# Performance work log

Hardware: AMD Instinct MI355X
Metric: run time of the kernel (lower is better)

## Reference

```python
import jax, jax.numpy as jnp
import numpy as np

B, N, E = 8, 20000, 320000
IN_F, EMBED, HIDDEN = 3, 64, 128


def setup_inputs() -> dict:
    key = jax.random.key(0)
    ks = jax.random.split(key, 16)
    w = lambda k, shape: (jax.random.normal(k, shape, jnp.float32) * 0.05)
    return {
        "actions": jax.random.normal(ks[0], (B, N, 2), jnp.float32),
        "node_features": jax.random.normal(ks[1], (B, 1, N), jnp.float32),
        "edge_index": jax.random.randint(ks[2], (B, 2, E), 0, N, dtype=jnp.int64),
        # GINConv 1 MLP: Linear(3, hidden) -> ReLU -> Linear(hidden, embed)
        "c1_w1": w(ks[3], (IN_F, HIDDEN)), "c1_b1": jnp.zeros((HIDDEN,), jnp.float32),
        "c1_w2": w(ks[4], (HIDDEN, EMBED)), "c1_b2": jnp.zeros((EMBED,), jnp.float32),
        # GINConv 2 MLP: Linear(embed, hidden) -> ReLU -> Linear(hidden, embed)
        "c2_w1": w(ks[5], (EMBED, HIDDEN)), "c2_b1": jnp.zeros((HIDDEN,), jnp.float32),
        "c2_w2": w(ks[6], (HIDDEN, EMBED)), "c2_b2": jnp.zeros((EMBED,), jnp.float32),
        # post-pool MLP (num_mlp_layers=1): Linear(embed, hidden)
        "mlp_w": w(ks[7], (EMBED, HIDDEN)), "mlp_b": jnp.zeros((HIDDEN,), jnp.float32),
        # output layer: Linear(hidden, num_nodes)
        "out_w": w(ks[8], (HIDDEN, N)), "out_b": jnp.zeros((N,), jnp.float32),
    }


def _gin_conv(x, src, dst, w1, b1, w2, b2):
    # message = x[src]; aggregate = scatter-sum into dst; eps=0 -> x + agg; then MLP
    num_nodes = x.shape[0]
    agg = jnp.zeros((num_nodes, x.shape[1]), x.dtype).at[dst].add(x[src])
    h = x + agg
    return jax.nn.relu(h @ w1 + b1) @ w2 + b2


def reference(actions, node_features, edge_index,
              c1_w1, c1_b1, c1_w2, c1_b2,
              c2_w1, c2_b1, c2_w2, c2_b2,
              mlp_w, mlp_b, out_w, out_b):
    nf = jnp.squeeze(node_features)                      # [B, N]
    x = jnp.stack((actions[:, :, 0], actions[:, :, 1], nf), axis=2)  # [B, N, 3]
    x = x.reshape(B * N, IN_F)
    # per-batch node-index offsets, then the original's row-major reshape to (2, B*E)
    offs = (jnp.arange(B, dtype=edge_index.dtype) * N)[:, None, None]
    ei = (edge_index + offs).reshape(2, B * E)
    src, dst = ei[0], ei[1]
    # conv layers (eval mode: dropout is identity), outer ReLU after each conv
    x = jax.nn.relu(_gin_conv(x, src, dst, c1_w1, c1_b1, c1_w2, c1_b2))
    x = jax.nn.relu(_gin_conv(x, src, dst, c2_w1, c2_b1, c2_w2, c2_b2))
    # global sum pool: batch ids are contiguous blocks of N nodes
    x = x.reshape(B, N, EMBED).sum(axis=1)               # [B, embed]
    x = jax.nn.relu(x @ mlp_w + mlp_b)                   # [B, hidden]
    return jax.nn.sigmoid(x @ out_w + out_b)             # [B, num_nodes]
```

## Files before the change

kernel.cpp:

```cpp
#include <hip/hip_runtime.h>
#include <cstdint>
#include <cstddef>

#define NBATCH 8
#define NNODE  20000
#define TWO_E  640000
#define NEDGE  2560000
#define BN     160000
#define HN     80000
#define HID    128
#define EMB    64

#define SB     5000
#define SBB    1250
#define NWG    320
#define CHUNK  8000
#define DCAP   80

#define OFF_POOL     0ull
#define ZERO_BYTES   2048ull
#define OFF_CNT      2048ull
#define OFF_TOTAL    6402048ull
#define OFF_BSTART   6422048ull
#define OFF_BINS     6442080ull
#define OFF_AGG1F    16682080ull
#define OFF_AGG2     17642080ull
#define OFF_X1       27882080ull
#define OFF_W1T1     48362080ull
#define OFF_W1HI     48363616ull
#define OFF_W2HI     48380000ull
#define OFF_W1LO     48396384ull
#define OFF_W2LO     48412768ull
#define OFF_V2HI     48429152ull
#define OFF_V2LO     48445536ull
#define OFF_Q        48461920ull

using bf16x8 = __attribute__((ext_vector_type(8))) short;
using f32x4  = __attribute__((ext_vector_type(4))) float;

__device__ __forceinline__ float bf2f(unsigned short u) {
    union { unsigned int i; float f; } v; v.i = ((unsigned int)u) << 16; return v.f;
}
__device__ __forceinline__ unsigned short f2bf(float x) {
    union { float f; unsigned int i; } v; v.f = x;
    unsigned int r = v.i + 0x7FFF + ((v.i >> 16) & 1);
    return (unsigned short)(r >> 16);
}
__device__ __forceinline__ unsigned int addbf2(unsigned int a, unsigned int b) {
    float lo = bf2f((unsigned short)(a & 0xFFFF)) + bf2f((unsigned short)(b & 0xFFFF));
    float hi = bf2f((unsigned short)(a >> 16))    + bf2f((unsigned short)(b >> 16));
    return (unsigned int)f2bf(lo) | ((unsigned int)f2bf(hi) << 16);
}
__device__ __forceinline__ int chunk_of(int b) { return (b & 7) * 40 + (b >> 3); }

__global__ void k_transpose(const float* __restrict__ w1, const float* __restrict__ v2,
                            const float* __restrict__ w2, const float* __restrict__ w2b,
                            float* __restrict__ w1t,
                            unsigned short* __restrict__ v2hi, unsigned short* __restrict__ v2lo,
                            unsigned short* __restrict__ w1hi, unsigned short* __restrict__ w1lo,
                            unsigned short* __restrict__ w2hi, unsigned short* __restrict__ w2lo) {
    int t = blockIdx.x * blockDim.x + threadIdx.x;
    int stride = gridDim.x * blockDim.x;
    for (int i = t; i < 3 * 128; i += stride) {
        int k = i / 128, j = i % 128;
        w1t[j * 3 + k] = w1[i];
    }
    for (int i = t; i < 8192; i += stride) {
        int j = i & 7, l = (i >> 3) & 63, fid = i >> 9;
        int n16 = fid >> 2, ks = fid & 3;
        int n = n16 * 16 + (l & 15), k = ks * 32 + (l >> 4) * 8 + j;
        float w = v2[k * 64 + n];
        unsigned short hi = f2bf(w);
        v2hi[i] = hi;
        v2lo[i] = f2bf(w - bf2f(hi));
    }
    for (int i = t; i < 8192; i += stride) {
        int j = i & 7, l = (i >> 3) & 63, fid = i >> 9;
        int n16 = fid >> 1, ks = fid & 1;
        int n = n16 * 16 + (l & 15), k = ks * 32 + (l >> 4) * 8 + j;
        float w = w2[k * 128 + n];
        unsigned short hi = f2bf(w);
        w1hi[i] = hi;
        w1lo[i] = f2bf(w - bf2f(hi));
    }
    for (int i = t; i < 8192; i += stride) {
        int j = i & 7, l = (i >> 3) & 63, fid = i >> 9;
        int n16 = fid >> 2, ks = fid & 3;
        int n = n16 * 16 + (l & 15), k = ks * 32 + (l >> 4) * 8 + j;
        float w = w2b[k * 64 + n];
        unsigned short hi = f2bf(w);
        w2hi[i] = hi;
        w2lo[i] = f2bf(w - bf2f(hi));
    }
}

__global__ __launch_bounds__(256) void k_hist(const int* __restrict__ ei,
                                              int* __restrict__ cnt) {
    __shared__ int hist[SB];
    int tid = threadIdx.x, w = chunk_of(blockIdx.x);
    for (int b = tid; b < SB; b += 256) hist[b] = 0;
    __syncthreads();
    for (int i = tid; i < CHUNK; i += 256) {
        int ig = w * CHUNK + i;
        int b = ig / TWO_E;
        int j = ig - b * TWO_E;
        int d4 = b * NNODE + ei[(b + 4) * TWO_E + j];
        atomicAdd(&hist[d4 >> 4], 1);
    }
    __syncthreads();
    for (int b = tid; b < SB; b += 256) cnt[w * SB + b] = hist[b];
}

__global__ __launch_bounds__(256) void k_scanA(int* __restrict__ cnt,
                                               int* __restrict__ total) {
    __shared__ int m[NWG][20];
    int tid = threadIdx.x;
    int b0 = blockIdx.x * 20;
    for (int i = tid; i < NWG * 20; i += 256) {
        int r = i / 20, c = i - r * 20;
        m[r][c] = cnt[r * SB + b0 + c];
    }
    __syncthreads();
    if (tid < 20) {
        int s = 0;
#pragma unroll 8
        for (int r = 0; r < NWG; ++r) { int v = m[r][tid]; m[r][tid] = s; s += v; }
        total[b0 + tid] = s;
    }
    __syncthreads();
    for (int i = tid; i < NWG * 20; i += 256) {
        int r = i / 20, c = i - r * 20;
        cnt[r * SB + b0 + c] = m[r][c];
    }
}

__global__ __launch_bounds__(1024) void k_scanB(const int* __restrict__ total,
                                                int* __restrict__ binStart) {
    __shared__ int tmp[1024];
    int tid = threadIdx.x;
    int v[5], c[5], s = 0;
    if (tid < 1000) {
#pragma unroll
        for (int k = 0; k < 5; ++k) v[k] = total[tid * 5 + k];
#pragma unroll
        for (int k = 0; k < 5; ++k) { c[k] = s; s += v[k]; }
    }
    tmp[tid] = s;
    __syncthreads();
    for (int off = 1; off < 1024; off <<= 1) {
        int t = (tid >= off) ? tmp[tid - off] : 0;
        __syncthreads();
        tmp[tid] += t;
        __syncthreads();
    }
    if (tid < 1000) {
        int excl = tmp[tid] - s;
#pragma unroll
        for (int k = 0; k < 5; ++k) binStart[tid * 5 + k] = excl + c[k];
    }
    if (tid == 0) binStart[SB] = NEDGE;
}

__global__ __launch_bounds__(256) void k_place(const int* __restrict__ ei,
                                               const int* __restrict__ cnt,
                                               const int* __restrict__ binStart,
                                               unsigned int* __restrict__ bins) {
    __shared__ int cur[SB];
    int tid = threadIdx.x, w = chunk_of(blockIdx.x);
    for (int b = tid; b < SB; b += 256) cur[b] = binStart[b] + cnt[w * SB + b];
    __syncthreads();
    for (int i = tid; i < CHUNK; i += 256) {
        int ig = w * CHUNK + i;
        int b = ig / TWO_E;
        int j = ig - b * TWO_E;
        int sn = ei[b * TWO_E + j];
        int d4 = b * NNODE + ei[(b + 4) * TWO_E + j];
        unsigned int e = ((unsigned int)d4 << 15) | (unsigned int)sn;
        int pos = atomicAdd(&cur[d4 >> 4], 1);
        bins[pos] = e;
    }
}

__global__ __launch_bounds__(256) void k_agg1(const unsigned int* __restrict__ bins,
                                              const int* __restrict__ binStart,
                                              const float* __restrict__ actions,
                                              const float* __restrict__ nf,
                                              float* __restrict__ agg1f) {
    int tid = threadIdx.x, lane = tid & 63, wv = tid >> 6;
    int sub = blockIdx.x * 4 + wv;
    int dstBase = sub * 16;
    int batchBase = (dstBase / NNODE) * NNODE;
    int start = binStart[sub];
    int cnt = binStart[sub + 1] - start;
    const float2* act2 = reinterpret_cast<const float2*>(actions);

    float acc[48];
#pragma unroll
    for (int k = 0; k < 48; ++k) acc[k] = 0.0f;

    for (int base = 0; base < cnt; base += 64) {
        int i = base + lane;
        float v0 = 0.f, v1 = 0.f, v2 = 0.f;
        int slot = 16;
        if (i < cnt) {
            unsigned int e = bins[start + i];
            slot = (int)((e >> 15) & 15);
            int s = batchBase + (int)(e & 0x7FFF);
            float2 a = act2[s];
            v0 = a.x; v1 = a.y; v2 = nf[s];
        }
#pragma unroll
        for (int t = 0; t < 16; ++t) {
            bool m = (slot == t);
            acc[t * 3 + 0] += m ? v0 : 0.0f;
            acc[t * 3 + 1] += m ? v1 : 0.0f;
            acc[t * 3 + 2] += m ? v2 : 0.0f;
        }
    }

#pragma unroll
    for (int k = 0; k < 48; ++k) {
        float v = acc[k];
        v += __shfl_xor(v, 1, 64);
        v += __shfl_xor(v, 2, 64);
        v += __shfl_xor(v, 4, 64);
        v += __shfl_xor(v, 8, 64);
        v += __shfl_xor(v, 16, 64);
        v += __shfl_xor(v, 32, 64);
        acc[k] = v;
    }
    float outv = 0.0f;
#pragma unroll
    for (int k = 0; k < 48; ++k) outv = (lane == k) ? acc[k] : outv;
    if (lane < 48) agg1f[dstBase * 3 + lane] = outv;
}

__global__ __launch_bounds__(256) void k_conv1(const float* __restrict__ actions,
                                               const float* __restrict__ nf,
                                               const float* __restrict__ agg1f,
                                               const float* __restrict__ w1t,
                                               const float* __restrict__ b1,
                                               const unsigned short* __restrict__ v2hi,
                                               const unsigned short* __restrict__ v2lo,
                                               const float* __restrict__ b2,
                                               unsigned short* __restrict__ x1) {
    __shared__ float hL[32][3];
    __shared__ __align__(16) unsigned short Hid[32][136];
    const int tid  = threadIdx.x;
    const int lane = tid & 63;
    const int wv   = tid >> 6;
    const int quad = lane >> 4;
    const int l16  = lane & 15;
    const int m0   = blockIdx.x * 32;

    if (tid < 32) {
        int t = m0 + tid;
        const float2* act2 = reinterpret_cast<const float2*>(actions);
        float2 a = act2[t];
        float h0 = a.x, h1 = a.y, h2 = nf[t];
        if (t >= HN) {
            int d4 = t - HN;
            h0 += agg1f[d4 * 3 + 0];
            h1 += agg1f[d4 * 3 + 1];
            h2 += agg1f[d4 * 3 + 2];
        }
        hL[tid][0] = h0; hL[tid][1] = h1; hL[tid][2] = h2;
    }
    __syncthreads();

    {
        int node = tid >> 3, jg = (tid & 7) * 16;
        float h0 = hL[node][0], h1 = hL[node][1], h2 = hL[node][2];
        float vv[16];
#pragma unroll
        for (int u = 0; u < 16; ++u) {
            int j = jg + u;
            vv[u] = fmaxf(fmaf(h0, w1t[3 * j + 0],
                          fmaf(h1, w1t[3 * j + 1],
                          fmaf(h2, w1t[3 * j + 2], b1[j]))), 0.0f);
        }
        uint4 A, B;
        A.x = (unsigned int)f2bf(vv[0])  | ((unsigned int)f2bf(vv[1])  << 16);
        A.y = (unsigned int)f2bf(vv[2])  | ((unsigned int)f2bf(vv[3])  << 16);
        A.z = (unsigned int)f2bf(vv[4])  | ((unsigned int)f2bf(vv[5])  << 16);
        A.w = (unsigned int)f2bf(vv[6])  | ((unsigned int)f2bf(vv[7])  << 16);
        B.x = (unsigned int)f2bf(vv[8])  | ((unsigned int)f2bf(vv[9])  << 16);
        B.y = (unsigned int)f2bf(vv[10]) | ((unsigned int)f2bf(vv[11]) << 16);
        B.z = (unsigned int)f2bf(vv[12]) | ((unsigned int)f2bf(vv[13]) << 16);
        B.w = (unsigned int)f2bf(vv[14]) | ((unsigned int)f2bf(vv[15]) << 16);
        *reinterpret_cast<uint4*>(&Hid[node][jg]) = A;
        *reinterpret_cast<uint4*>(&Hid[node][jg + 8]) = B;
    }
    __syncthreads();

    {
        const int mt = wv & 1;
        const int nb = (wv >> 1) * 32;
        f32x4 acc[2];
#pragma unroll
        for (int nt = 0; nt < 2; ++nt) acc[nt] = {0.f, 0.f, 0.f, 0.f};
#pragma unroll
        for (int ks = 0; ks < 4; ++ks) {
            bf16x8 a = *reinterpret_cast<const bf16x8*>(&Hid[mt * 16 + l16][ks * 32 + quad * 8]);
#pragma unroll
            for (int nt = 0; nt < 2; ++nt) {
                int fid = ((nb >> 4) + nt) * 4 + ks;
                bf16x8 whi = *reinterpret_cast<const bf16x8*>(&v2hi[(size_t)(fid * 64 + lane) * 8]);
                bf16x8 wlo = *reinterpret_cast<const bf16x8*>(&v2lo[(size_t)(fid * 64 + lane) * 8]);
                acc[nt] = __builtin_amdgcn_mfma_f32_16x16x32_bf16(a, whi, acc[nt], 0, 0, 0);
                acc[nt] = __builtin_amdgcn_mfma_f32_16x16x32_bf16(a, wlo, acc[nt], 0, 0, 0);
            }
        }
#pragma unroll
        for (int nt = 0; nt < 2; ++nt) {
            int n = nb + nt * 16 + l16;
            float bias = b2[n];
#pragma unroll
            for (int r = 0; r < 4; ++r) {
                int node = mt * 16 + quad * 4 + r;
                x1[(size_t)(m0 + node) * 64 + n] = f2bf(fmaxf(acc[nt][r] + bias, 0.0f));
            }
        }
    }
}

__global__ __launch_bounds__(256) void k_agg2(const unsigned int* __restrict__ bins,
                                              const int* __restrict__ binStart,
                                              const unsigned short* __restrict__ x1,
                                              unsigned short* __restrict__ agg2) {
    __shared__ unsigned int seg[4][8 * DCAP];
    int tid = threadIdx.x, lane = tid & 63, wv = tid >> 6;
    int xcd = blockIdx.x & 7, jj = blockIdx.x >> 3;
    int batch = xcd >> 1, halfB = xcd & 1;
    int local = jj * 2 + (wv >> 1);
    if (local >= 625) return;
    int sub = batch * SBB + halfB * 625 + local;
    int halfD = wv & 1;
    int dstBase = sub * 16 + halfD * 8;
    int batchBase = batch * NNODE;
    unsigned int* myseg = seg[wv];

    int start = binStart[sub];
    int cnt = binStart[sub + 1] - start;

    int cur[8];
#pragma unroll
    for (int t = 0; t < 8; ++t) cur[t] = 0;
    for (int base = 0; base < cnt; base += 64) {
        int i = base + lane;
        int slot = 8;
        unsigned int e = 0;
        if (i < cnt) {
            e = bins[start + i];
            int s = (int)((e >> 15) & 15) - halfD * 8;
            slot = ((unsigned)s < 8u) ? s : 8;
        }
        int pos = DCAP;
        int st = 8;
#pragma unroll
        for (int t = 0; t < 8; ++t) {
            unsigned long long mask = __ballot(slot == t);
            int rank = (int)__popcll(mask & ((1ull << lane) - 1ull));
            bool m = (slot == t);
            pos = m ? (cur[t] + rank) : pos;
            st  = m ? t : st;
            cur[t] += (int)__popcll(mask);
        }
        if (st < 8 && pos < DCAP) myseg[st * DCAP + pos] = e;
    }

#pragma unroll 1
    for (int t = 0; t < 8; ++t) {
        int n = cur[t]; if (n > DCAP) n = DCAP;
        int base = t * DCAP;
        float a0 = 0.f, a1 = 0.f, a2 = 0.f, a3 = 0.f;
        int p = 0;
        for (; p + 4 <= n; p += 4) {
            unsigned int e0 = myseg[base + p],     e1 = myseg[base + p + 1];
            unsigned int e2 = myseg[base + p + 2], e3 = myseg[base + p + 3];
            int s0 = batchBase + (int)(e0 & 0x7FFF);
            int s1 = batchBase + (int)(e1 & 0x7FFF);
            int s2 = batchBase + (int)(e2 & 0x7FFF);
            int s3 = batchBase + (int)(e3 & 0x7FFF);
            a0 += bf2f(x1[(size_t)s0 * 64 + lane]);
            a1 += bf2f(x1[(size_t)s1 * 64 + lane]);
            a2 += bf2f(x1[(size_t)s2 * 64 + lane]);
            a3 += bf2f(x1[(size_t)s3 * 64 + lane]);
        }
        for (; p < n; ++p) {
            unsigned int e0 = myseg[base + p];
            int s0 = batchBase + (int)(e0 & 0x7FFF);
            a0 += bf2f(x1[(size_t)s0 * 64 + lane]);
        }
        agg2[(size_t)(dstBase + t) * 64 + lane] = f2bf((a0 + a1) + (a2 + a3));
    }
}

__global__ __launch_bounds__(256) void k_conv2pool(const unsigned short* __restrict__ x1,
                                                   const unsigned short* __restrict__ agg2,
                                                   const unsigned short* __restrict__ w1hi,
                                                   const unsigned short* __restrict__ w1lo,
                                                   const unsigned short* __restrict__ w2hi,
                                                   const unsigned short* __restrict__ w2lo,
                                                   const float* __restrict__ b1,
                                                   const float* __restrict__ b2,
                                                   float* __restrict__ pool) {
    __shared__ __align__(16) unsigned short Hs[32][72];
    __shared__ __align__(16) unsigned short Hid[32][136];
    __shared__ float poolLDS[64];

    const int tid  = threadIdx.x;
    const int lane = tid & 63;
    const int wv   = tid >> 6;
    const int quad = lane >> 4;
    const int l16  = lane & 15;

    const int m0 = blockIdx.x * 32;
    const int b  = m0 / NNODE;
    const int mt = wv & 1;

    if (tid < 64) poolLDS[tid] = 0.0f;

    {
        int row = tid >> 3, g = tid & 7;
        const uint4* xr = reinterpret_cast<const uint4*>(x1 + (size_t)(m0 + row) * 64 + g * 8);
        uint4 v = *xr;
        if (m0 >= HN) {
            const uint4* ar = reinterpret_cast<const uint4*>(agg2 + (size_t)(m0 - HN + row) * 64 + g * 8);
            uint4 a = *ar;
            v.x = addbf2(v.x, a.x); v.y = addbf2(v.y, a.y);
            v.z = addbf2(v.z, a.z); v.w = addbf2(v.w, a.w);
        }
        *reinterpret_cast<uint4*>(&Hs[row][g * 8]) = v;
    }
    __syncthreads();

    {
        const int nb = (wv >> 1) * 64;
        f32x4 acc[4];
#pragma unroll
        for (int nt = 0; nt < 4; ++nt) acc[nt] = {0.f, 0.f, 0.f, 0.f};
#pragma unroll
        for (int ks = 0; ks < 2; ++ks) {
            bf16x8 h = *reinterpret_cast<const bf16x8*>(&Hs[mt * 16 + l16][ks * 32 + quad * 8]);
#pragma unroll
            for (int nt = 0; nt < 4; ++nt) {
                int fid = ((nb >> 4) + nt) * 2 + ks;
                bf16x8 whi = *reinterpret_cast<const bf16x8*>(&w1hi[(size_t)(fid * 64 + lane) * 8]);
                bf16x8 wlo = *reinterpret_cast<const bf16x8*>(&w1lo[(size_t)(fid * 64 + lane) * 8]);
                acc[nt] = __builtin_amdgcn_mfma_f32_16x16x32_bf16(whi, h, acc[nt], 0, 0, 0);
                acc[nt] = __builtin_amdgcn_mfma_f32_16x16x32_bf16(wlo, h, acc[nt], 0, 0, 0);
            }
        }
#pragma unroll
        for (int nt = 0; nt < 4; ++nt) {
            int hbase = nb + nt * 16 + quad * 4;
            float4 bias = *reinterpret_cast<const float4*>(&b1[hbase]);
            unsigned int p0 = (unsigned int)f2bf(fmaxf(acc[nt][0] + bias.x, 0.0f))
                            | ((unsigned int)f2bf(fmaxf(acc[nt][1] + bias.y, 0.0f)) << 16);
            unsigned int p1 = (unsigned int)f2bf(fmaxf(acc[nt][2] + bias.z, 0.0f))
                            | ((unsigned int)f2bf(fmaxf(acc[nt][3] + bias.w, 0.0f)) << 16);
            uint2 pk; pk.x = p0; pk.y = p1;
            *reinterpret_cast<uint2*>(&Hid[mt * 16 + l16][hbase]) = pk;
        }
    }
    __syncthreads();

    {
        const int nb = (wv >> 1) * 32;
        f32x4 acc[2];
#pragma unroll
        for (int nt = 0; nt < 2; ++nt) acc[nt] = {0.f, 0.f, 0.f, 0.f};
#pragma unroll
        for (int ks = 0; ks < 4; ++ks) {
            bf16x8 a = *reinterpret_cast<const bf16x8*>(&Hid[mt * 16 + l16][ks * 32 + quad * 8]);
#pragma unroll
            for (int nt = 0; nt < 2; ++nt) {
                int fid = ((nb >> 4) + nt) * 4 + ks;
                bf16x8 whi = *reinterpret_cast<const bf16x8*>(&w2hi[(size_t)(fid * 64 + lane) * 8]);
                bf16x8 wlo = *reinterpret_cast<const bf16x8*>(&w2lo[(size_t)(fid * 64 + lane) * 8]);
                acc[nt] = __builtin_amdgcn_mfma_f32_16x16x32_bf16(a, whi, acc[nt], 0, 0, 0);
                acc[nt] = __builtin_amdgcn_mfma_f32_16x16x32_bf16(a, wlo, acc[nt], 0, 0, 0);
            }
        }
#pragma unroll
        for (int nt = 0; nt < 2; ++nt) {
            int n = nb + nt * 16 + l16;
            float bias = b2[n];
            float p = 0.0f;
#pragma unroll
            for (int r = 0; r < 4; ++r) p += fmaxf(acc[nt][r] + bias, 0.0f);
            p += __shfl_xor(p, 16, 64);
            p += __shfl_xor(p, 32, 64);
            if (lane < 16) atomicAdd(&poolLDS[n], p);
        }
    }
    __syncthreads();

    if (tid < 64) atomicAdd(&pool[b * 64 + tid], poolLDS[tid]);
}

__global__ __launch_bounds__(128) void k_q(const float* __restrict__ pool,
                                           const float* __restrict__ mlp_w,
                                           const float* __restrict__ mlp_b,
                                           float* __restrict__ q) {
    int j = threadIdx.x;
    for (int b = 0; b < NBATCH; ++b) {
        float a = mlp_b[j];
#pragma unroll 8
        for (int k = 0; k < 64; ++k) a = fmaf(pool[b * 64 + k], mlp_w[k * 128 + j], a);
        q[b * 128 + j] = fmaxf(a, 0.0f);
    }
}

__global__ __launch_bounds__(256) void k_out(const float* __restrict__ q,
                                             const float* __restrict__ out_w,
                                             const float* __restrict__ out_b,
                                             float* __restrict__ out) {
    __shared__ float qs[NBATCH][128];
    int tid = threadIdx.x;
    for (int i = tid; i < NBATCH * 128; i += 256) qs[i >> 7][i & 127] = q[i];
    __syncthreads();
    int c = tid & 31, b = tid >> 5;
    int n = blockIdx.x * 32 + c;
    const float* qr = qs[b];
    float a = out_b[n];
#pragma unroll 8
    for (int j = 0; j < 128; ++j) a = fmaf(qr[j], out_w[j * NNODE + n], a);
    out[b * NNODE + n] = 1.0f / (1.0f + expf(-a));
}

extern "C" void kernel_launch(void* const* d_in, const int* in_sizes, int n_in,
                              void* d_out, int out_size, void* d_ws, size_t ws_size,
                              hipStream_t stream) {
    const float* actions = (const float*)d_in[0];
    const float* nf      = (const float*)d_in[1];
    const int*   ei      = (const int*)d_in[2];
    const float* c1_w1   = (const float*)d_in[3];
    const float* c1_b1   = (const float*)d_in[4];
    const float* c1_w2   = (const float*)d_in[5];
    const float* c1_b2   = (const float*)d_in[6];
    const float* c2_w1   = (const float*)d_in[7];
    const float* c2_b1   = (const float*)d_in[8];
    const float* c2_w2   = (const float*)d_in[9];
    const float* c2_b2   = (const float*)d_in[10];
    const float* mlp_w   = (const float*)d_in[11];
    const float* mlp_b   = (const float*)d_in[12];
    const float* out_w   = (const float*)d_in[13];
    const float* out_b   = (const float*)d_in[14];
    float* out = (float*)d_out;

    char* ws = (char*)d_ws;
    float*        pool     = (float*)(ws + OFF_POOL);
    int*          cnt      = (int*)(ws + OFF_CNT);
    int*          total    = (int*)(ws + OFF_TOTAL);
    int*          binStart = (int*)(ws + OFF_BSTART);
    unsigned int* bins     = (unsigned int*)(ws + OFF_BINS);
    float*        agg1f    = (float*)(ws + OFF_AGG1F);
    unsigned short* agg2   = (unsigned short*)(ws + OFF_AGG2);
    unsigned short* x1     = (unsigned short*)(ws + OFF_X1);
    float* w1t1 = (float*)(ws + OFF_W1T1);
    unsigned short* w1hi = (unsigned short*)(ws + OFF_W1HI);
    unsigned short* w2hi = (unsigned short*)(ws + OFF_W2HI);
    unsigned short* w1lo = (unsigned short*)(ws + OFF_W1LO);
    unsigned short* w2lo = (unsigned short*)(ws + OFF_W2LO);
    unsigned short* v2hi = (unsigned short*)(ws + OFF_V2HI);
    unsigned short* v2lo = (unsigned short*)(ws + OFF_V2LO);
    float* q = (float*)(ws + OFF_Q);

    hipMemsetAsync(d_ws, 0, ZERO_BYTES, stream);

    k_transpose<<<32, 256, 0, stream>>>(c1_w1, c1_w2, c2_w1, c2_w2,
                                        w1t1, v2hi, v2lo, w1hi, w1lo, w2hi, w2lo);

    k_hist <<<NWG, 256, 0, stream>>>(ei, cnt);
    k_scanA<<<SB / 20, 256, 0, stream>>>(cnt, total);
    k_scanB<<<1, 1024, 0, stream>>>(total, binStart);
    k_place<<<NWG, 256, 0, stream>>>(ei, cnt, binStart, bins);

    k_agg1<<<SB / 4, 256, 0, stream>>>(bins, binStart, actions, nf, agg1f);
    k_conv1<<<BN / 32, 256, 0, stream>>>(actions, nf, agg1f, w1t1, c1_b1,
                                         v2hi, v2lo, c1_b2, x1);
    k_agg2<<<2560, 256, 0, stream>>>(bins, binStart, x1, agg2);

    k_conv2pool<<<BN / 32, 256, 0, stream>>>(x1, agg2, w1hi, w1lo, w2hi, w2lo,
                                             c2_b1, c2_b2, pool);

    k_q<<<1, 128, 0, stream>>>(pool, mlp_w, mlp_b, q);
    k_out<<<NNODE / 32, 256, 0, stream>>>(q, out_w, out_b, out);
}
```

Measured before the change: 359.3 us.

## Fuse layer-2 edge aggregation into conv2pool and interleave heavy/light blocks

Removes the separate k_agg2 kernel and its bf16 agg2 buffer by performing the bin-based gather-sum directly inside k_conv2pool, writing the aggregated row into shared memory before the MFMA layers. Blocks are remapped so aggregation-heavy tiles (batches 4-7) alternate with light ones (batches 0-3) across XCDs, balancing work. It also stores pre-shifted source offsets in LDS and sums in fp32 before a single bf16 rounding. Cost: conv2pool blocks now carry irregular gather latency and extra LDS, which may reduce occupancy.

Result: slower. 395.6 us (+10.1%).

```diff
diff --git a/kernel.cpp b/kernel.cpp
--- a/kernel.cpp
+++ b/kernel.cpp
@@ -24,16 +24,15 @@
 #define OFF_BSTART   6422048ull
 #define OFF_BINS     6442080ull
 #define OFF_AGG1F    16682080ull
-#define OFF_AGG2     17642080ull
-#define OFF_X1       27882080ull
-#define OFF_W1T1     48362080ull
-#define OFF_W1HI     48363616ull
-#define OFF_W2HI     48380000ull
-#define OFF_W1LO     48396384ull
-#define OFF_W2LO     48412768ull
-#define OFF_V2HI     48429152ull
-#define OFF_V2LO     48445536ull
-#define OFF_Q        48461920ull
+#define OFF_X1       17642080ull
+#define OFF_W1T1     38122080ull
+#define OFF_W1HI     38123616ull
+#define OFF_W2HI     38140000ull
+#define OFF_W1LO     38156384ull
+#define OFF_W2LO     38172768ull
+#define OFF_V2HI     38189152ull
+#define OFF_V2LO     38205536ull
+#define OFF_Q        38221920ull
 
 using bf16x8 = __attribute__((ext_vector_type(8))) short;
 using f32x4  = __attribute__((ext_vector_type(4))) float;
@@ -45,11 +44,6 @@
     union { float f; unsigned int i; } v; v.f = x;
     unsigned int r = v.i + 0x7FFF + ((v.i >> 16) & 1);
     return (unsigned short)(r >> 16);
-}
-__device__ __forceinline__ unsigned int addbf2(unsigned int a, unsigned int b) {
-    float lo = bf2f((unsigned short)(a & 0xFFFF)) + bf2f((unsigned short)(b & 0xFFFF));
-    float hi = bf2f((unsigned short)(a >> 16))    + bf2f((unsigned short)(b >> 16));
-    return (unsigned int)f2bf(lo) | ((unsigned int)f2bf(hi) << 16);
 }
 __device__ __forceinline__ int chunk_of(int b) { return (b & 7) * 40 + (b >> 3); }
 
@@ -324,80 +318,9 @@
     }
 }
 
-__global__ __launch_bounds__(256) void k_agg2(const unsigned int* __restrict__ bins,
-                                              const int* __restrict__ binStart,
-                                              const unsigned short* __restrict__ x1,
-                                              unsigned short* __restrict__ agg2) {
-    __shared__ unsigned int seg[4][8 * DCAP];
-    int tid = threadIdx.x, lane = tid & 63, wv = tid >> 6;
-    int xcd = blockIdx.x & 7, jj = blockIdx.x >> 3;
-    int batch = xcd >> 1, halfB = xcd & 1;
-    int local = jj * 2 + (wv >> 1);
-    if (local >= 625) return;
-    int sub = batch * SBB + halfB * 625 + local;
-    int halfD = wv & 1;
-    int dstBase = sub * 16 + halfD * 8;
-    int batchBase = batch * NNODE;
-    unsigned int* myseg = seg[wv];
-
-    int start = binStart[sub];
-    int cnt = binStart[sub + 1] - start;
-
-    int cur[8];
-#pragma unroll
-    for (int t = 0; t < 8; ++t) cur[t] = 0;
-    for (int base = 0; base < cnt; base += 64) {
-        int i = base + lane;
-        int slot = 8;
-        unsigned int e = 0;
-        if (i < cnt) {
-            e = bins[start + i];
-            int s = (int)((e >> 15) & 15) - halfD * 8;
-            slot = ((unsigned)s < 8u) ? s : 8;
-        }
-        int pos = DCAP;
-        int st = 8;
-#pragma unroll
-        for (int t = 0; t < 8; ++t) {
-            unsigned long long mask = __ballot(slot == t);
-            int rank = (int)__popcll(mask & ((1ull << lane) - 1ull));
-            bool m = (slot == t);
-            pos = m ? (cur[t] + rank) : pos;
-            st  = m ? t : st;
-            cur[t] += (int)__popcll(mask);
-        }
-        if (st < 8 && pos < DCAP) myseg[st * DCAP + pos] = e;
-    }
-
-#pragma unroll 1
-    for (int t = 0; t < 8; ++t) {
-        int n = cur[t]; if (n > DCAP) n = DCAP;
-        int base = t * DCAP;
-        float a0 = 0.f, a1 = 0.f, a2 = 0.f, a3 = 0.f;
-        int p = 0;
-        for (; p + 4 <= n; p += 4) {
-            unsigned int e0 = myseg[base + p],     e1 = myseg[base + p + 1];
-            unsigned int e2 = myseg[base + p + 2], e3 = myseg[base + p + 3];
-            int s0 = batchBase + (int)(e0 & 0x7FFF);
-            int s1 = batchBase + (int)(e1 & 0x7FFF);
-            int s2 = batchBase + (int)(e2 & 0x7FFF);
-            int s3 = batchBase + (int)(e3 & 0x7FFF);
-            a0 += bf2f(x1[(size_t)s0 * 64 + lane]);
-            a1 += bf2f(x1[(size_t)s1 * 64 + lane]);
-            a2 += bf2f(x1[(size_t)s2 * 64 + lane]);
-            a3 += bf2f(x1[(size_t)s3 * 64 + lane]);
-        }
-        for (; p < n; ++p) {
-            unsigned int e0 = myseg[base + p];
-            int s0 = batchBase + (int)(e0 & 0x7FFF);
-            a0 += bf2f(x1[(size_t)s0 * 64 + lane]);
-        }
-        agg2[(size_t)(dstBase + t) * 64 + lane] = f2bf((a0 + a1) + (a2 + a3));
-    }
-}
-
-__global__ __launch_bounds__(256) void k_conv2pool(const unsigned short* __restrict__ x1,
-                                                   const unsigned short* __restrict__ agg2,
+__global__ __launch_bounds__(256) void k_conv2pool(const unsigned int* __restrict__ bins,
+                                                   const int* __restrict__ binStart,
+                                                   const unsigned short* __restrict__ x1,
                                                    const unsigned short* __restrict__ w1hi,
                                                    const unsigned short* __restrict__ w1lo,
                                                    const unsigned short* __restrict__ w2hi,
@@ -405,6 +328,7 @@
                                                    const float* __restrict__ b1,
                                                    const float* __restrict__ b2,
                                                    float* __restrict__ pool) {
+    __shared__ unsigned int seg[4][8 * DCAP];
     __shared__ __align__(16) unsigned short Hs[32][72];
     __shared__ __align__(16) unsigned short Hid[32][136];
     __shared__ float poolLDS[64];
@@ -415,23 +339,77 @@
     const int quad = lane >> 4;
     const int l16  = lane & 15;
 
-    const int m0 = blockIdx.x * 32;
-    const int b  = m0 / NNODE;
+    const int xcd = blockIdx.x & 7;
+    const int i   = blockIdx.x >> 3;
+    const int k   = xcd >> 1;
+    const int h   = xcd & 1;
+    const bool heavy = (((i ^ h) & 1) == 0);
+    const int b  = heavy ? (4 + k) : k;
+    const int m0 = b * NNODE + i * 32;
     const int mt = wv & 1;
 
     if (tid < 64) poolLDS[tid] = 0.0f;
 
-    {
+    if (heavy) {
+        int d4b = k * NNODE + i * 32 + wv * 8;
+        int sub = d4b >> 4;
+        int halfD = (d4b >> 3) & 1;
+        int batchBase = k * NNODE;
+        unsigned int* myseg = seg[wv];
+        int start = binStart[sub];
+        int cnt = binStart[sub + 1] - start;
+
+        int cur[8];
+#pragma unroll
+        for (int t = 0; t < 8; ++t) cur[t] = 0;
+        for (int base = 0; base < cnt; base += 64) {
+            int idx = base + lane;
+            int slot = 8;
+            unsigned int payload = 0;
+            if (idx < cnt) {
+                unsigned int e = bins[start + idx];
+                int s = (int)((e >> 15) & 15) - halfD * 8;
+                slot = ((unsigned)s < 8u) ? s : 8;
+                payload = (e & 0x7FFFu) << 6;
+            }
+            int pos = DCAP;
+            int st = 8;
+#pragma unroll
+            for (int t = 0; t < 8; ++t) {
+                unsigned long long mask = __ballot(slot == t);
+                int rank = (int)__popcll(mask & ((1ull << lane) - 1ull));
+                bool m = (slot == t);
+                pos = m ? (cur[t] + rank) : pos;
+                st  = m ? t : st;
+                cur[t] += (int)__popcll(mask);
+            }
+            if (st < 8 && pos < DCAP) myseg[st * DCAP + pos] = payload;
+        }
+
+        const unsigned short* xb = x1 + (size_t)batchBase * 64 + lane;
+#pragma unroll 1
+        for (int t = 0; t < 8; ++t) {
+            int n = cur[t]; if (n > DCAP) n = DCAP;
+            int base = t * DCAP;
+            float a0 = 0.f, a1 = 0.f, a2 = 0.f, a3 = 0.f;
+            int p = 0;
+            for (; p + 4 <= n; p += 4) {
+                unsigned int o0 = myseg[base + p],     o1 = myseg[base + p + 1];
+                unsigned int o2 = myseg[base + p + 2], o3 = myseg[base + p + 3];
+                a0 += bf2f(xb[o0]);
+                a1 += bf2f(xb[o1]);
+                a2 += bf2f(xb[o2]);
+                a3 += bf2f(xb[o3]);
+            }
+            for (; p < n; ++p) a0 += bf2f(xb[myseg[base + p]]);
+            int row = wv * 8 + t;
+            float own = bf2f(x1[(size_t)(m0 + row) * 64 + lane]);
+            Hs[row][lane] = f2bf(((a0 + a1) + (a2 + a3)) + own);
+        }
+    } else {
         int row = tid >> 3, g = tid & 7;
         const uint4* xr = reinterpret_cast<const uint4*>(x1 + (size_t)(m0 + row) * 64 + g * 8);
-        uint4 v = *xr;
-        if (m0 >= HN) {
-            const uint4* ar = reinterpret_cast<const uint4*>(agg2 + (size_t)(m0 - HN + row) * 64 + g * 8);
-            uint4 a = *ar;
-            v.x = addbf2(v.x, a.x); v.y = addbf2(v.y, a.y);
-            v.z = addbf2(v.z, a.z); v.w = addbf2(v.w, a.w);
-        }
-        *reinterpret_cast<uint4*>(&Hs[row][g * 8]) = v;
+        *reinterpret_cast<uint4*>(&Hs[row][g * 8]) = *xr;
     }
     __syncthreads();
 
@@ -442,14 +420,14 @@
         for (int nt = 0; nt < 4; ++nt) acc[nt] = {0.f, 0.f, 0.f, 0.f};
 #pragma unroll
         for (int ks = 0; ks < 2; ++ks) {
-            bf16x8 h = *reinterpret_cast<const bf16x8*>(&Hs[mt * 16 + l16][ks * 32 + quad * 8]);
+            bf16x8 hh = *reinterpret_cast<const bf16x8*>(&Hs[mt * 16 + l16][ks * 32 + quad * 8]);
 #pragma unroll
             for (int nt = 0; nt < 4; ++nt) {
                 int fid = ((nb >> 4) + nt) * 2 + ks;
                 bf16x8 whi = *reinterpret_cast<const bf16x8*>(&w1hi[(size_t)(fid * 64 + lane) * 8]);
                 bf16x8 wlo = *reinterpret_cast<const bf16x8*>(&w1lo[(size_t)(fid * 64 + lane) * 8]);
-                acc[nt] = __builtin_amdgcn_mfma_f32_16x16x32_bf16(whi, h, acc[nt], 0, 0, 0);
-                acc[nt] = __builtin_amdgcn_mfma_f32_16x16x32_bf16(wlo, h, acc[nt], 0, 0, 0);
+                acc[nt] = __builtin_amdgcn_mfma_f32_16x16x32_bf16(whi, hh, acc[nt], 0, 0, 0);
+                acc[nt] = __builtin_amdgcn_mfma_f32_16x16x32_bf16(wlo, hh, acc[nt], 0, 0, 0);
             }
         }
 #pragma unroll
@@ -557,7 +535,6 @@
     int*          binStart = (int*)(ws + OFF_BSTART);
     unsigned int* bins     = (unsigned int*)(ws + OFF_BINS);
     float*        agg1f    = (float*)(ws + OFF_AGG1F);
-    unsigned short* agg2   = (unsigned short*)(ws + OFF_AGG2);
     unsigned short* x1     = (unsigned short*)(ws + OFF_X1);
     float* w1t1 = (float*)(ws + OFF_W1T1);
     unsigned short* w1hi = (unsigned short*)(ws + OFF_W1HI);
@@ -581,9 +558,8 @@
     k_agg1<<<SB / 4, 256, 0, stream>>>(bins, binStart, actions, nf, agg1f);
     k_conv1<<<BN / 32, 256, 0, stream>>>(actions, nf, agg1f, w1t1, c1_b1,
                                          v2hi, v2lo, c1_b2, x1);
-    k_agg2<<<2560, 256, 0, stream>>>(bins, binStart, x1, agg2);
-
-    k_conv2pool<<<BN / 32, 256, 0, stream>>>(x1, agg2, w1hi, w1lo, w2hi, w2lo,
+    k_conv2pool<<<BN / 32, 256, 0, stream>>>(bins, binStart, x1,
+                                             w1hi, w1lo, w2hi, w2lo,
                                              c2_b1, c2_b2, pool);
 
     k_q<<<1, 128, 0, stream>>>(pool, mlp_w, mlp_b, q);
```
